# Kernel tuning notes

Measured on AMD Instinct MI355X. Metric: run time of the kernel, lower is better.

## Reference

```python
import jax, jax.numpy as jnp
import numpy as np
import math

MAXL = 2
N = 256
TAU = 8


def _cg_coeff(j1, m1, j2, m2, J, M):
    if m1 + m2 != M or J < abs(j1 - j2) or J > j1 + j2:
        return 0.0
    f = math.factorial
    pre = math.sqrt((2 * J + 1) * f(J + j1 - j2) * f(J - j1 + j2) * f(j1 + j2 - J) / f(j1 + j2 + J + 1))
    pre *= math.sqrt(f(J + M) * f(J - M) * f(j1 - m1) * f(j1 + m1) * f(j2 - m2) * f(j2 + m2))
    kmin = max(0, j2 - J - m1, j1 + m2 - J)
    kmax = min(j1 + j2 - J, j1 - m1, j2 + m2)
    s = 0.0
    for k in range(kmin, kmax + 1):
        s += (-1.0) ** k / (f(k) * f(j1 + j2 - J - k) * f(j1 - m1 - k) * f(j2 + m2 - k) * f(J - j2 + m1 + k) * f(J - j1 - m2 + k))
    return pre * s


def _cg_tensor(l1, l2, L):
    C = np.zeros((2 * l1 + 1, 2 * l2 + 1, 2 * L + 1), np.float32)
    for m1 in range(-l1, l1 + 1):
        for m2 in range(-l2, l2 + 1):
            M = m1 + m2
            if -L <= M <= L:
                C[m1 + l1, m2 + l2, M + L] = _cg_coeff(l1, m1, l2, m2, L, M)
    return C

_CG = {}
for _l1 in range(MAXL + 1):
    for _l2 in range(MAXL + 1):
        for _L in range(abs(_l1 - _l2), min(_l1 + _l2, MAXL) + 1):
            _CG[(_l1, _l2, _L)] = _cg_tensor(_l1, _l2, _L)


def _cgproduct(xs, ys, maxl):
    # xs[l]: [..., 2l+1, tau_x], ys[l]: [..., 2l+1, tau_y]
    out = []
    for L in range(maxl + 1):
        chunks = []
        for l1 in range(maxl + 1):
            for l2 in range(maxl + 1):
                if abs(l1 - l2) <= L <= l1 + l2:
                    C = jnp.asarray(_CG[(l1, l2, L)])
                    t = jnp.einsum('...mc,...nd,mnM->...Mcd', xs[l1], ys[l2], C)
                    sh = t.shape
                    chunks.append(t.reshape(sh[:-2] + (sh[-2] * sh[-1],)))
        out.append(jnp.concatenate(chunks, axis=-1))
    return out


def _forward(v0, v1, v2, adj, s0, s1, s2, wn0, wn1, wn2, wr0, wr1, wr2):
    v = [v0, v1, v2]                       # [N, 1, 2l+1, tau]
    sph = [s0[None], s1[None], s2[None]]   # [1, N, N, 2l+1, 1]
    wn = [wn0, wn1, wn2]
    wr = [wr0, wr1, wr2]
    # message pass: gather/sum over neighbors (Rmask1 gather)
    vmp = [jnp.einsum('ij,jamc->iamc', adj, p)[None] for p in v]  # [1, N, 1, 2l+1, tau]
    # first CG product (vertex x vertex)
    cg_nl = _cgproduct(vmp, vmp, MAXL)
    # per-l channel mixing with weights_nl
    mixed = [jnp.einsum('bxymc,cd->bxymd', cg_nl[l], wn[l]) for l in range(MAXL + 1)]
    # repeat to pairwise adims [N, N] (broadcast over second array dim)
    n = adj.shape[0]
    rep = [jnp.broadcast_to(m, (1, n, n, m.shape[3], m.shape[4])) for m in mixed]
    # second CG product with relative-position spherical harmonics
    cg_rel = _cgproduct(rep, sph, MAXL)
    # per-cell mixing with weights_rel
    mixed_rel = [jnp.einsum('bxymc,xycd->bxymd', cg_rel[l], wr[l]) for l in range(MAXL + 1)]
    # sum over source-node array dim
    vsum = [jnp.sum(m, axis=1) for m in mixed_rel]  # [1, N, 2l+1, tau]
    # NormalizeVecArr mutates parts in place -> returned vertices_sum is normalized
    out = [p / jnp.sum(p) for p in vsum]
    # concatenate parts along m-axis for a single output array [1, N, 9, tau]
    return jnp.concatenate(out, axis=2)


def setup_inputs() -> dict:
    key = jax.random.key(0)
    ks = jax.random.split(key, 13)
    d = {}
    d['v0'] = jax.random.normal(ks[0], (N, 1, 1, TAU), jnp.float32)
    d['v1'] = jax.random.normal(ks[1], (N, 1, 3, TAU), jnp.float32)
    d['v2'] = jax.random.normal(ks[2], (N, 1, 5, TAU), jnp.float32)
    d['adj'] = jax.random.uniform(ks[3], (N, N), jnp.float32)
    d['s0'] = jax.random.normal(ks[4], (N, N, 1, 1), jnp.float32)
    d['s1'] = jax.random.normal(ks[5], (N, N, 3, 1), jnp.float32)
    d['s2'] = jax.random.normal(ks[6], (N, N, 5, 1), jnp.float32)
    W = 0.05
    d['wn0'] = W * jax.random.normal(ks[7], (192, TAU), jnp.float32)
    d['wn1'] = W * jax.random.normal(ks[8], (384, TAU), jnp.float32)
    d['wn2'] = W * jax.random.normal(ks[9], (384, TAU), jnp.float32)
    d['wr0'] = W * jax.random.normal(ks[10], (N, N, 24, TAU), jnp.float32)
    d['wr1'] = W * jax.random.normal(ks[11], (N, N, 48, TAU), jnp.float32)
    d['wr2'] = W * jax.random.normal(ks[12], (N, N, 48, TAU), jnp.float32)
    return d


def reference(v0, v1, v2, adj, s0, s1, s2, wn0, wn1, wn2, wr0, wr1, wr2):
    return _forward(v0, v1, v2, adj, s0, s1, s2, wn0, wn1, wn2, wr0, wr1, wr2)
```

## Files before the change

kernel.cpp:

```cpp
#include <hip/hip_runtime.h>

#define NN 256
#define XPW 4

#define C13  0.5773502691896258f
#define C15  0.4472135954999579f
#define CC12 0.7071067811865476f
#define S35  0.7745966692414834f
#define S310 0.5477225575051661f
#define C110 0.3162277660168379f
#define S25  0.6324555320336759f
#define S23  0.8164965809277260f
#define C16  0.4082482904638630f
#define S27  0.5345224838248488f
#define S37  0.6546536707079771f
#define C114 0.2672612419124244f

#define CGREL(mx, sv, r0, r1, r2) \
    r0[0] = mx[0]*sv[0]; \
    r0[1] = C13*(mx[1]*sv[3] - mx[2]*sv[2] + mx[3]*sv[1]); \
    r0[2] = C15*(mx[4]*sv[8] - mx[5]*sv[7] + mx[6]*sv[6] - mx[7]*sv[5] + mx[8]*sv[4]); \
    r1[0][0] = mx[0]*sv[1]; r1[1][0] = mx[0]*sv[2]; r1[2][0] = mx[0]*sv[3]; \
    r1[0][1] = mx[1]*sv[0]; r1[1][1] = mx[2]*sv[0]; r1[2][1] = mx[3]*sv[0]; \
    r1[0][2] = CC12*(mx[2]*sv[1] - mx[1]*sv[2]); \
    r1[1][2] = CC12*(mx[3]*sv[1] - mx[1]*sv[3]); \
    r1[2][2] = CC12*(mx[3]*sv[2] - mx[2]*sv[3]); \
    r1[0][3] = S35*mx[3]*sv[4] - S310*mx[2]*sv[5] + C110*mx[1]*sv[6]; \
    r1[1][3] = S310*(mx[3]*sv[5] + mx[1]*sv[7]) - S25*mx[2]*sv[6]; \
    r1[2][3] = S35*mx[1]*sv[8] - S310*mx[2]*sv[7] + C110*mx[3]*sv[6]; \
    r1[0][4] = C110*mx[6]*sv[1] - S310*mx[5]*sv[2] + S35*mx[4]*sv[3]; \
    r1[1][4] = S310*(mx[7]*sv[1] + mx[5]*sv[3]) - S25*mx[6]*sv[2]; \
    r1[2][4] = S35*mx[8]*sv[1] - S310*mx[7]*sv[2] + C110*mx[6]*sv[3]; \
    r1[0][5] = C15*(mx[7]*sv[4] - mx[4]*sv[7]) + S310*(mx[5]*sv[6] - mx[6]*sv[5]); \
    r1[1][5] = S25*(mx[8]*sv[4] - mx[4]*sv[8]) + C110*(mx[5]*sv[7] - mx[7]*sv[5]); \
    r1[2][5] = C15*(mx[8]*sv[5] - mx[5]*sv[8]) + S310*(mx[6]*sv[7] - mx[7]*sv[6]); \
    r2[0][0]=mx[0]*sv[4]; r2[1][0]=mx[0]*sv[5]; r2[2][0]=mx[0]*sv[6]; r2[3][0]=mx[0]*sv[7]; r2[4][0]=mx[0]*sv[8]; \
    r2[0][1] = mx[1]*sv[1]; \
    r2[1][1] = CC12*(mx[2]*sv[1] + mx[1]*sv[2]); \
    r2[2][1] = C16*(mx[3]*sv[1] + mx[1]*sv[3]) + S23*mx[2]*sv[2]; \
    r2[3][1] = CC12*(mx[3]*sv[2] + mx[2]*sv[3]); \
    r2[4][1] = mx[3]*sv[3]; \
    r2[0][2] = S23*mx[2]*sv[4] - C13*mx[1]*sv[5]; \
    r2[1][2] = C13*mx[3]*sv[4] + C16*mx[2]*sv[5] - CC12*mx[1]*sv[6]; \
    r2[2][2] = CC12*(mx[3]*sv[5] - mx[1]*sv[7]); \
    r2[3][2] = CC12*mx[3]*sv[6] - C16*mx[2]*sv[7] - C13*mx[1]*sv[8]; \
    r2[4][2] = C13*mx[3]*sv[7] - S23*mx[2]*sv[8]; \
    r2[0][3]=mx[4]*sv[0]; r2[1][3]=mx[5]*sv[0]; r2[2][3]=mx[6]*sv[0]; r2[3][3]=mx[7]*sv[0]; r2[4][3]=mx[8]*sv[0]; \
    r2[0][4] = C13*mx[5]*sv[1] - S23*mx[4]*sv[2]; \
    r2[1][4] = CC12*mx[6]*sv[1] - C16*mx[5]*sv[2] - C13*mx[4]*sv[3]; \
    r2[2][4] = CC12*(mx[7]*sv[1] - mx[5]*sv[3]); \
    r2[3][4] = C13*mx[8]*sv[1] + C16*mx[7]*sv[2] - CC12*mx[6]*sv[3]; \
    r2[4][4] = S23*mx[8]*sv[2] - C13*mx[7]*sv[3]; \
    r2[0][5] = S27*(mx[4]*sv[6] + mx[6]*sv[4]) - S37*mx[5]*sv[5]; \
    r2[1][5] = S37*(mx[4]*sv[7] + mx[7]*sv[4]) - C114*(mx[5]*sv[6] + mx[6]*sv[5]); \
    r2[2][5] = S27*(mx[8]*sv[4] + mx[4]*sv[8] - mx[6]*sv[6]) + C114*(mx[7]*sv[5] + mx[5]*sv[7]); \
    r2[3][5] = S37*(mx[8]*sv[5] + mx[5]*sv[8]) - C114*(mx[7]*sv[6] + mx[6]*sv[7]); \
    r2[4][5] = S27*(mx[8]*sv[6] + mx[6]*sv[8]) - S37*mx[7]*sv[7];

__global__ __launch_bounds__(256) void k_nodes(
                        const float* __restrict__ adj,
                        const float* __restrict__ v0,
                        const float* __restrict__ v1,
                        const float* __restrict__ v2,
                        const float* __restrict__ wn0,
                        const float* __restrict__ wn1,
                        const float* __restrict__ wn2,
                        float* __restrict__ mixed){
  __shared__ float part[4][72];
  int i = blockIdx.x;
  int tid = threadIdx.x, wv = tid >> 6, lane = tid & 63;
  {
    const float* vp1; int st1;
    if (lane < 8)       { vp1 = v0 + lane;      st1 = 8;  }
    else if (lane < 32) { vp1 = v1 + (lane-8);  st1 = 24; }
    else                { vp1 = v2 + (lane-32); st1 = 40; }
    const float* vp2 = v2 + 32 + lane;
    const float* arow = adj + i*NN;
    int j0 = wv*64;
    float a1a = 0.f, a1b = 0.f, a2a = 0.f, a2b = 0.f;
    #pragma unroll 8
    for (int j = j0; j < j0+64; j += 2){
      float av0 = arow[j], av1 = arow[j+1];
      a1a = fmaf(av0, vp1[j*st1], a1a);
      a1b = fmaf(av1, vp1[(j+1)*st1], a1b);
      if (lane < 8){
        a2a = fmaf(av0, vp2[j*40], a2a);
        a2b = fmaf(av1, vp2[(j+1)*40], a2b);
      }
    }
    part[wv][lane] = a1a + a1b;
    if (lane < 8) part[wv][64+lane] = a2a + a2b;
  }
  __syncthreads();
  if (wv) return;
  {
    float s = part[0][lane] + part[1][lane] + part[2][lane] + part[3][lane];
    float s2 = 0.f;
    if (lane < 8)
      s2 = part[0][64+lane] + part[1][64+lane] + part[2][64+lane] + part[3][64+lane];
    part[0][lane] = s;
    if (lane < 8) part[0][64+lane] = s2;
  }
  int c = lane >> 3, d = lane & 7;
  float mx[9], sv[9];
  #pragma unroll
  for (int j=0;j<9;j++){ mx[j] = part[0][j*8 + c]; sv[j] = part[0][j*8 + d]; }
  float r0[3], r1[3][6], r2[5][6];
  CGREL(mx, sv, r0, r1, r2)

  float a0[8], a1m[3][8], a2m[5][8];
  #pragma unroll
  for (int dp=0;dp<8;dp++){ a0[dp]=0.f;
    #pragma unroll
    for (int M=0;M<3;M++) a1m[M][dp]=0.f;
    #pragma unroll
    for (int M=0;M<5;M++) a2m[M][dp]=0.f;
  }
  #pragma unroll
  for (int k=0;k<3;k++){
    const float* row = wn0 + (k*64 + lane)*8;
    float4 u = *(const float4*)row;
    float4 v = *(const float4*)(row+4);
    float u8[8] = {u.x,u.y,u.z,u.w,v.x,v.y,v.z,v.w};
    #pragma unroll
    for (int dp=0;dp<8;dp++) a0[dp] = fmaf(r0[k], u8[dp], a0[dp]);
  }
  #pragma unroll
  for (int k=0;k<6;k++){
    const float* row = wn1 + (k*64 + lane)*8;
    float4 u = *(const float4*)row;
    float4 v = *(const float4*)(row+4);
    float u8[8] = {u.x,u.y,u.z,u.w,v.x,v.y,v.z,v.w};
    #pragma unroll
    for (int M=0;M<3;M++)
      #pragma unroll
      for (int dp=0;dp<8;dp++) a1m[M][dp] = fmaf(r1[M][k], u8[dp], a1m[M][dp]);
  }
  #pragma unroll
  for (int k=0;k<6;k++){
    const float* row = wn2 + (k*64 + lane)*8;
    float4 u = *(const float4*)row;
    float4 v = *(const float4*)(row+4);
    float u8[8] = {u.x,u.y,u.z,u.w,v.x,v.y,v.z,v.w};
    #pragma unroll
    for (int M=0;M<5;M++)
      #pragma unroll
      for (int dp=0;dp<8;dp++) a2m[M][dp] = fmaf(r2[M][k], u8[dp], a2m[M][dp]);
  }
  #pragma unroll
  for (int m=0;m<9;m++){
    #pragma unroll
    for (int dp=0;dp<8;dp++){
      float val = (m==0) ? a0[dp] : (m<4 ? a1m[m-1][dp] : a2m[m-4][dp]);
      val += __shfl_xor(val, 1);
      val += __shfl_xor(val, 2);
      val += __shfl_xor(val, 4);
      val += __shfl_xor(val, 8);
      val += __shfl_xor(val, 16);
      val += __shfl_xor(val, 32);
      if (lane == ((m*8+dp) & 63)) mixed[i*72 + m*8 + dp] = val;
    }
  }
}

__global__ __launch_bounds__(256) void k_pair(
    const float* __restrict__ mixed,
    const float* __restrict__ s0, const float* __restrict__ s1, const float* __restrict__ s2,
    const float* __restrict__ wr0, const float* __restrict__ wr1, const float* __restrict__ wr2,
    float* __restrict__ vsum){
  __shared__ float red[4][72];
  int tid = threadIdx.x;
  int wv = tid >> 6, lane = tid & 63;
  int y = blockIdx.x & (NN-1);
  int xsel = blockIdx.x >> 8;
  int xbase = (xsel*4 + wv) * XPW;
  int cgp = lane >> 3;

  float acc[9];
  #pragma unroll
  for (int m=0;m<9;m++) acc[m]=0.f;

  #pragma unroll
  for (int i=0;i<XPW;i++){
    int x = xbase + i;
    int pxy = x*NN + y;
    const float* p0 = wr0 + (size_t)pxy*192 + lane;
    const float* p1 = wr1 + (size_t)pxy*384 + lane;
    const float* p2 = wr2 + (size_t)pxy*384 + lane;
    float w0v[3], w1v[6], w2v[6];
    #pragma unroll
    for (int k=0;k<3;k++) w0v[k] = __builtin_nontemporal_load(p0 + k*64);
    #pragma unroll
    for (int k=0;k<6;k++) w1v[k] = __builtin_nontemporal_load(p1 + k*64);
    #pragma unroll
    for (int k=0;k<6;k++) w2v[k] = __builtin_nontemporal_load(p2 + k*64);

    float mx[9], sv[9];
    {
      const float* mb = mixed + x*72 + cgp;
      #pragma unroll
      for (int j=0;j<9;j++) mx[j] = mb[j*8];
      sv[0] = s0[pxy];
      #pragma unroll
      for (int j=0;j<3;j++) sv[1+j] = s1[(size_t)pxy*3+j];
      #pragma unroll
      for (int j=0;j<5;j++) sv[4+j] = s2[(size_t)pxy*5+j];
    }

    float r0[3], r1[3][6], r2[5][6];
    CGREL(mx, sv, r0, r1, r2)

    #pragma unroll
    for (int k=0;k<3;k++) acc[0] = fmaf(r0[k], w0v[k], acc[0]);
    #pragma unroll
    for (int k=0;k<6;k++){
      acc[1] = fmaf(r1[0][k], w1v[k], acc[1]);
      acc[2] = fmaf(r1[1][k], w1v[k], acc[2]);
      acc[3] = fmaf(r1[2][k], w1v[k], acc[3]);
      acc[4] = fmaf(r2[0][k], w2v[k], acc[4]);
      acc[5] = fmaf(r2[1][k], w2v[k], acc[5]);
      acc[6] = fmaf(r2[2][k], w2v[k], acc[6]);
      acc[7] = fmaf(r2[3][k], w2v[k], acc[7]);
      acc[8] = fmaf(r2[4][k], w2v[k], acc[8]);
    }
  }

  #pragma unroll
  for (int m=0;m<9;m++){
    float v = acc[m];
    v += __shfl_xor(v, 8);
    v += __shfl_xor(v, 16);
    v += __shfl_xor(v, 32);
    acc[m] = v;
  }
  if (lane < 8){
    #pragma unroll
    for (int m=0;m<9;m++) red[wv][m*8+lane] = acc[m];
  }
  __syncthreads();
  if (tid < 72){
    float v = red[0][tid] + red[1][tid] + red[2][tid] + red[3][tid];
    atomicAdd(&vsum[y*72 + tid], v);
  }
}

__global__ void k_final(const float* __restrict__ vsum, float* __restrict__ out){
  __shared__ float ps[3];
  int t = threadIdx.x;
  if (t < 3) ps[t] = 0.f;
  __syncthreads();
  float vals[18];
  float p0=0.f, p1=0.f, p2=0.f;
  #pragma unroll
  for (int k=0;k<18;k++){
    int idx = t*18 + k;
    float v = vsum[idx];
    vals[k] = v;
    int mall = (idx >> 3) % 9;
    if (mall == 0) p0 += v; else if (mall < 4) p1 += v; else p2 += v;
  }
  #pragma unroll
  for (int s=1; s<64; s<<=1){
    p0 += __shfl_xor(p0, s);
    p1 += __shfl_xor(p1, s);
    p2 += __shfl_xor(p2, s);
  }
  if ((t & 63) == 0){
    atomicAdd(&ps[0], p0);
    atomicAdd(&ps[1], p1);
    atomicAdd(&ps[2], p2);
  }
  __syncthreads();
  float q0 = ps[0], q1 = ps[1], q2 = ps[2];
  #pragma unroll
  for (int k=0;k<18;k++){
    int idx = t*18 + k;
    int mall = (idx >> 3) % 9;
    float den = (mall == 0) ? q0 : (mall < 4 ? q1 : q2);
    out[idx] = vals[k] / den;
  }
}

extern "C" void kernel_launch(void* const* d_in, const int* in_sizes, int n_in,
                              void* d_out, int out_size, void* d_ws, size_t ws_size,
                              hipStream_t stream) {
  const float* v0  = (const float*)d_in[0];
  const float* v1  = (const float*)d_in[1];
  const float* v2  = (const float*)d_in[2];
  const float* adj = (const float*)d_in[3];
  const float* s0  = (const float*)d_in[4];
  const float* s1  = (const float*)d_in[5];
  const float* s2  = (const float*)d_in[6];
  const float* wn0 = (const float*)d_in[7];
  const float* wn1 = (const float*)d_in[8];
  const float* wn2 = (const float*)d_in[9];
  const float* wr0 = (const float*)d_in[10];
  const float* wr1 = (const float*)d_in[11];
  const float* wr2 = (const float*)d_in[12];
  float* out = (float*)d_out;

  float* ws    = (float*)d_ws;
  float* mixed = ws;
  float* vsum  = ws + 18432;

  hipMemsetAsync(vsum, 0, 18432*sizeof(float), stream);
  k_nodes<<<NN, 256, 0, stream>>>(adj, v0, v1, v2, wn0, wn1, wn2, mixed);
  k_pair<<<NN*16, 256, 0, stream>>>(mixed, s0, s1, s2, wr0, wr1, wr2, vsum);
  k_final<<<1, 1024, 0, stream>>>(vsum, out);
}
```

Baseline: 83.68 us.

## Replace atomic vsum with per-slice partials and parallel final normalization

```diff
diff --git a/kernel.cpp b/kernel.cpp
--- a/kernel.cpp
+++ b/kernel.cpp
@@ -1,7 +1,8 @@
 #include <hip/hip_runtime.h>
 
 #define NN 256
-#define XPW 4
+#define XPW 8
+#define NXS (NN/(4*XPW))
 
 #define C13  0.5773502691896258f
 #define C15  0.4472135954999579f
@@ -65,10 +66,12 @@
                         const float* __restrict__ wn0,
                         const float* __restrict__ wn1,
                         const float* __restrict__ wn2,
-                        float* __restrict__ mixed){
+                        float* __restrict__ mixed,
+                        float* __restrict__ psum){
   __shared__ float part[4][72];
   int i = blockIdx.x;
   int tid = threadIdx.x, wv = tid >> 6, lane = tid & 63;
+  if (i == 0 && tid < 3) psum[tid] = 0.f;
   {
     const float* vp1; int st1;
     if (lane < 8)       { vp1 = v0 + lane;      st1 = 8;  }
@@ -167,8 +170,9 @@
     const float* __restrict__ mixed,
     const float* __restrict__ s0, const float* __restrict__ s1, const float* __restrict__ s2,
     const float* __restrict__ wr0, const float* __restrict__ wr1, const float* __restrict__ wr2,
-    float* __restrict__ vsum){
+    float* __restrict__ part, float* __restrict__ psum){
   __shared__ float red[4][72];
+  __shared__ float bp[3];
   int tid = threadIdx.x;
   int wv = tid >> 6, lane = tid & 63;
   int y = blockIdx.x & (NN-1);
@@ -180,7 +184,6 @@
   #pragma unroll
   for (int m=0;m<9;m++) acc[m]=0.f;
 
-  #pragma unroll
   for (int i=0;i<XPW;i++){
     int x = xbase + i;
     int pxy = x*NN + y;
@@ -237,48 +240,31 @@
     #pragma unroll
     for (int m=0;m<9;m++) red[wv][m*8+lane] = acc[m];
   }
+  if (tid < 3) bp[tid] = 0.f;
   __syncthreads();
   if (tid < 72){
     float v = red[0][tid] + red[1][tid] + red[2][tid] + red[3][tid];
-    atomicAdd(&vsum[y*72 + tid], v);
-  }
-}
-
-__global__ void k_final(const float* __restrict__ vsum, float* __restrict__ out){
-  __shared__ float ps[3];
-  int t = threadIdx.x;
-  if (t < 3) ps[t] = 0.f;
+    part[((size_t)xsel*NN + y)*72 + tid] = v;
+    int mall = tid >> 3;
+    int l = (mall==0) ? 0 : (mall < 4 ? 1 : 2);
+    atomicAdd(&bp[l], v);
+  }
   __syncthreads();
-  float vals[18];
-  float p0=0.f, p1=0.f, p2=0.f;
-  #pragma unroll
-  for (int k=0;k<18;k++){
-    int idx = t*18 + k;
-    float v = vsum[idx];
-    vals[k] = v;
-    int mall = (idx >> 3) % 9;
-    if (mall == 0) p0 += v; else if (mall < 4) p1 += v; else p2 += v;
-  }
-  #pragma unroll
-  for (int s=1; s<64; s<<=1){
-    p0 += __shfl_xor(p0, s);
-    p1 += __shfl_xor(p1, s);
-    p2 += __shfl_xor(p2, s);
-  }
-  if ((t & 63) == 0){
-    atomicAdd(&ps[0], p0);
-    atomicAdd(&ps[1], p1);
-    atomicAdd(&ps[2], p2);
-  }
-  __syncthreads();
-  float q0 = ps[0], q1 = ps[1], q2 = ps[2];
-  #pragma unroll
-  for (int k=0;k<18;k++){
-    int idx = t*18 + k;
-    int mall = (idx >> 3) % 9;
-    float den = (mall == 0) ? q0 : (mall < 4 ? q1 : q2);
-    out[idx] = vals[k] / den;
-  }
+  if (tid < 3) atomicAdd(&psum[tid], bp[tid]);
+}
+
+__global__ __launch_bounds__(256) void k_final(
+    const float* __restrict__ part, const float* __restrict__ psum,
+    float* __restrict__ out){
+  int idx = blockIdx.x*256 + threadIdx.x;
+  int y = idx / 72;
+  int t = idx - y*72;
+  float v = 0.f;
+  #pragma unroll
+  for (int x=0; x<NXS; x++) v += part[((size_t)x*NN + y)*72 + t];
+  int mall = t >> 3;
+  float den = (mall == 0) ? psum[0] : (mall < 4 ? psum[1] : psum[2]);
+  out[idx] = v / den;
 }
 
 extern "C" void kernel_launch(void* const* d_in, const int* in_sizes, int n_in,
@@ -301,10 +287,10 @@
 
   float* ws    = (float*)d_ws;
   float* mixed = ws;
-  float* vsum  = ws + 18432;
-
-  hipMemsetAsync(vsum, 0, 18432*sizeof(float), stream);
-  k_nodes<<<NN, 256, 0, stream>>>(adj, v0, v1, v2, wn0, wn1, wn2, mixed);
-  k_pair<<<NN*16, 256, 0, stream>>>(mixed, s0, s1, s2, wr0, wr1, wr2, vsum);
-  k_final<<<1, 1024, 0, stream>>>(vsum, out);
-}
+  float* part  = ws + 18432;
+  float* psum  = ws + 18432 + 147456;
+
+  k_nodes<<<NN, 256, 0, stream>>>(adj, v0, v1, v2, wn0, wn1, wn2, mixed, psum);
+  k_pair<<<NN*NXS, 256, 0, stream>>>(mixed, s0, s1, s2, wr0, wr1, wr2, part, psum);
+  k_final<<<72, 256, 0, stream>>>(part, psum, out);
+}
```

After: 79.73 us, median of 2. 4.7% less time.
